# Optimization experiments

Measured on AMD Instinct MI355X. Metric: run time of the kernel, lower is better.

## Reference

```python
import jax, jax.numpy as jnp
import numpy as np

E = 2048        # embedding_dim
H = 16          # num_q_heads
G = 4           # group_size
HKV = H // G    # num_kv_heads = 4
D = E // H      # q_head_dim = 128
KVD = E // G    # kv_head_dim = 512
B, N = 2, 2048


def setup_inputs() -> dict:
    key = jax.random.key(0)
    ks = jax.random.split(key, 5)
    s = 0.02
    return {
        "x": jax.random.normal(ks[0], (B, N, E), jnp.float32),
        "Wq": jax.random.normal(ks[1], (E, E), jnp.float32) * s,
        "Wk": jax.random.normal(ks[2], (KVD, E), jnp.float32) * s,
        "Wv": jax.random.normal(ks[3], (KVD, E), jnp.float32) * s,
        "Wo": jax.random.normal(ks[4], (E, E), jnp.float32) * s,
    }


def reference(x, Wq, Wk, Wv, Wo):
    b, n, _ = x.shape
    # projections (nn.Linear: y = x @ W.T)
    q = x @ Wq.T                              # (b, n, E)
    k = x @ Wk.T                              # (b, n, KVD)
    v = x @ Wv.T                              # (b, n, KVD)
    # split heads: q -> b h n d with h=H, then (h g) -> g,h layout
    q = q.reshape(b, n, H, D).transpose(0, 2, 1, 3)          # b H n d
    q = q.reshape(b, HKV, G, n, D).transpose(0, 2, 1, 3, 4)  # b g h n d  (h=HKV)
    k = k.reshape(b, n, HKV, D).transpose(0, 2, 1, 3)        # b h s d
    v = v.reshape(b, n, HKV, D).transpose(0, 2, 1, 3)        # b h s d
    scale = 1.0 / jnp.sqrt(jnp.asarray(D, x.dtype))
    scores = jnp.einsum('bghnd,bhsd->bghns', q, k) * scale   # full score tensor
    scores = jax.nn.softmax(scores, axis=-1)
    # dropout p=0.0 -> identity
    o = jnp.einsum('bghns,bhsd->bghnd', scores, v)           # b g h n d
    # rearrange 'b g h n d -> b n (h g) d' then concat heads
    o = o.transpose(0, 3, 2, 1, 4).reshape(b, n, E)          # b n (h g) d -> b n E
    return o @ Wo.T
```

## Files before the change

### kernel.cpp

```cpp
#include <hip/hip_runtime.h>
#include <hip/hip_bf16.h>
#include <cstdint>
#include <cstddef>

using u16 = unsigned short;
typedef __bf16 bf16x8 __attribute__((ext_vector_type(8)));
typedef float f32x4 __attribute__((ext_vector_type(4)));
typedef float f32x16 __attribute__((ext_vector_type(16)));
typedef u16 u16x4 __attribute__((ext_vector_type(4)));
typedef u16 u16x8 __attribute__((ext_vector_type(8)));
typedef uint32_t u32x4 __attribute__((ext_vector_type(4)));

__device__ __forceinline__ u16 f2bf(float f) {
  uint32_t u = __builtin_bit_cast(uint32_t, f);
  u += 0x7FFFu + ((u >> 16) & 1u);
  return (u16)(u >> 16);
}

__device__ __forceinline__ void gld_lds16(const void* g, void* l) {
  __builtin_amdgcn_global_load_lds(
      (const __attribute__((address_space(1))) unsigned int*)g,
      (__attribute__((address_space(3))) unsigned int*)l, 16, 0, 0);
}

#define MFMA16(a, b, c) __builtin_amdgcn_mfma_f32_16x16x32_bf16((a), (b), (c), 0, 0, 0)
#define MFMA32(a, b, c) __builtin_amdgcn_mfma_f32_32x32x16_bf16((a), (b), (c), 0, 0, 0)

__device__ __forceinline__ uint32_t pkbf(float a, float b) {
  uint32_t d;
  asm("v_cvt_pk_bf16_f32 %0, %1, %2" : "=v"(d) : "v"(a), "v"(b));
  return d;
}
__device__ __forceinline__ void swap32(uint32_t& a, uint32_t& b) {
  asm volatile("v_permlane32_swap_b32 %0, %1" : "+v"(a), "+v"(b));
}

__global__ void cvt_kernel(const float* __restrict__ in, u16* __restrict__ out, int n4) {
  int i = blockIdx.x * blockDim.x + threadIdx.x;
  int stride = gridDim.x * blockDim.x;
  for (; i < n4; i += stride) {
    float4 v = reinterpret_cast<const float4*>(in)[i];
    u16x4 o;
    o[0] = f2bf(v.x); o[1] = f2bf(v.y); o[2] = f2bf(v.z); o[3] = f2bf(v.w);
    reinterpret_cast<u16x4*>(out)[i] = o;
  }
}

template <bool OUT_BF16>
__global__ __launch_bounds__(256) void gemm_bt(const u16* __restrict__ A,
                                               const u16* __restrict__ B,
                                               void* __restrict__ Cv,
                                               int M, int N, int K) {
  __shared__ __align__(16) u16 Ash[3][128 * 32];
  __shared__ __align__(16) u16 Bsh[3][128 * 32];
  const int tid = threadIdx.x;
  const int w = tid >> 6, lane = tid & 63, ql = lane & 15, g = lane >> 4;
  const int wr = w >> 1, wc = w & 1;
  const int m0 = blockIdx.y * 128, n0 = blockIdx.x * 128;
  const int srow = w * 16 + (lane >> 2);
  const int sk = (lane & 3) * 8;
  const u16* Abase = A + (size_t)(m0 + srow) * K + sk;
  const u16* Bbase = B + (size_t)(n0 + srow) * K + sk;

  f32x4 acc[4][4];
#pragma unroll
  for (int i = 0; i < 4; i++)
#pragma unroll
    for (int j = 0; j < 4; j++) acc[i][j] = f32x4{0.f, 0.f, 0.f, 0.f};

  auto stage = [&](int bi, int tile) {
    const int kt = tile * 32;
    gld_lds16(Abase + kt,                  &Ash[bi][w * 512]);
    gld_lds16(Abase + (size_t)64 * K + kt, &Ash[bi][2048 + w * 512]);
    gld_lds16(Bbase + kt,                  &Bsh[bi][w * 512]);
    gld_lds16(Bbase + (size_t)64 * K + kt, &Bsh[bi][2048 + w * 512]);
  };

  const int nt = K >> 5;
  stage(0, 0);
  stage(1, 1);
  asm volatile("s_waitcnt vmcnt(4)" ::: "memory");
  __builtin_amdgcn_sched_barrier(0);
  __builtin_amdgcn_s_barrier();
  __builtin_amdgcn_sched_barrier(0);

  int cur = 0;
  for (int t = 0; t < nt; ++t) {
    if (t + 2 < nt) {
      int stg = cur + 2; if (stg >= 3) stg -= 3;
      stage(stg, t + 2);
    }
    bf16x8 af[4], bfr[4];
#pragma unroll
    for (int i = 0; i < 4; i++)
      af[i] = *reinterpret_cast<const bf16x8*>(&Ash[cur][(wr * 64 + i * 16 + ql) * 32 + g * 8]);
#pragma unroll
    for (int j = 0; j < 4; j++)
      bfr[j] = *reinterpret_cast<const bf16x8*>(&Bsh[cur][(wc * 64 + j * 16 + ql) * 32 + g * 8]);
    __builtin_amdgcn_s_setprio(1);
#pragma unroll
    for (int i = 0; i < 4; i++)
#pragma unroll
      for (int j = 0; j < 4; j++)
        acc[i][j] = MFMA16(af[i], bfr[j], acc[i][j]);
    __builtin_amdgcn_s_setprio(0);
    if (t + 1 < nt) {
      if (t + 2 < nt) {
        asm volatile("s_waitcnt vmcnt(4)" ::: "memory");
      } else {
        asm volatile("s_waitcnt vmcnt(0)" ::: "memory");
      }
      __builtin_amdgcn_sched_barrier(0);
      __builtin_amdgcn_s_barrier();
      __builtin_amdgcn_sched_barrier(0);
    }
    cur = (cur == 2) ? 0 : cur + 1;
  }

#pragma unroll
  for (int i = 0; i < 4; i++)
#pragma unroll
    for (int j = 0; j < 4; j++)
#pragma unroll
      for (int r = 0; r < 4; r++) {
        const int row = m0 + wr * 64 + i * 16 + g * 4 + r;
        const int col = n0 + wc * 64 + j * 16 + ql;
        if constexpr (OUT_BF16)
          ((u16*)Cv)[(size_t)row * N + col] = f2bf(acc[i][j][r]);
        else
          ((float*)Cv)[(size_t)row * N + col] = acc[i][j][r];
      }
}

__global__ __launch_bounds__(256, 2) void attn_kernel(const u16* __restrict__ QKV,
                                                      u16* __restrict__ O) {
  __shared__ __align__(16) u16 Kb[2][64 * 128];
  __shared__ __align__(16) u16 Vb[2][2][128 * 32];
  const int tid = threadIdx.x, w = tid >> 6, lane = tid & 63;
  const int lq = lane & 31, hi = lane >> 5;
  const int qt = blockIdx.x;
  const int b = blockIdx.y >> 4, h = blockIdx.y & 15, hkv = h >> 2;
  const size_t rowb = (size_t)b * 2048;
  const int qbase = qt * 128 + w * 32;

  const u16* Kg = QKV + 2048 + hkv * 128;
  const u16* Vg = QKV + 2560 + hkv * 128;

  bf16x8 bq[8];
  {
    const u16* qp = QKV + (rowb + qbase + lq) * 3072 + h * 128 + hi * 8;
#pragma unroll
    for (int s5 = 0; s5 < 8; s5++)
      bq[s5] = *reinterpret_cast<const bf16x8*>(qp + s5 * 16);
  }

  const int dg = tid & 7, sl = tid >> 3;

  f32x16 oacc[4];
#pragma unroll
  for (int dt = 0; dt < 4; dt++)
#pragma unroll
    for (int i = 0; i < 16; i++) oacc[dt][i] = 0.f;
  float m = -INFINITY, l = 0.f;
  const float CEXP = 0.08838834764831845f * 1.4426950408889634f;

  auto stageK = [&](int pb2, int sbase) {
#pragma unroll
    for (int p = 0; p < 4; p++) {
      const int L = p * 2048 + tid * 8;
      const int s = L >> 7;
      const int gI = (L >> 3) & 15;
      gld_lds16(Kg + (rowb + sbase + s) * 3072 + ((gI ^ (s & 7)) << 3),
                &Kb[pb2][p * 2048 + w * 512]);
    }
  };
  auto writeV = [&](int pb2, const u16x8& a00, const u16x8& a01,
                    const u16x8& a10, const u16x8& a11) {
#pragma unroll
    for (int sh2 = 0; sh2 < 2; sh2++)
#pragma unroll
      for (int hf = 0; hf < 2; hf++) {
        const u16x8 v = sh2 ? (hf ? a11 : a10) : (hf ? a01 : a00);
#pragma unroll
        for (int j = 0; j < 8; j++) {
          const int d = dg * 16 + hf * 8 + j;
          const int key = ((d >> 1) ^ (d >> 4)) & 3;
          Vb[pb2][sh2][d * 32 + (sl ^ (key << 3))] = v[j];
        }
      }
  };

#define KFRAG(PB, SH, S5) \
  (*reinterpret_cast<const bf16x8*>(&Kb[PB][((SH)*32 + lq) * 128 + ((((S5)*2 + hi) ^ (lq & 7)) << 3)]))
#define VFRAG(PB, DT, SS) \
  (*reinterpret_cast<const bf16x8*>(&Vb[PB][(SS) >> 1][((DT)*32 + lq) * 32 + \
      ((((SS) & 1) * 16 + hi * 8) ^ (((((DT)*32 + lq) >> 1) ^ (((DT)*32 + lq) >> 4)) & 3) << 3)]))

  u16x8 v00, v01, v10, v11;
  {
    const u16* vp = Vg + (rowb + sl) * 3072 + dg * 16;
    v00 = *reinterpret_cast<const u16x8*>(vp);
    v01 = *reinterpret_cast<const u16x8*>(vp + 8);
    const u16* vp2 = vp + (size_t)32 * 3072;
    v10 = *reinterpret_cast<const u16x8*>(vp2);
    v11 = *reinterpret_cast<const u16x8*>(vp2 + 8);
  }
  stageK(0, 0);
  writeV(0, v00, v01, v10, v11);
  __syncthreads();

#pragma unroll 1
  for (int sb = 0; sb < 32; sb++) {
    const int pb = sb & 1;
    if (sb < 31) {
      const u16* vp = Vg + (rowb + (sb + 1) * 64 + sl) * 3072 + dg * 16;
      v00 = *reinterpret_cast<const u16x8*>(vp);
      v01 = *reinterpret_cast<const u16x8*>(vp + 8);
      const u16* vp2 = vp + (size_t)32 * 3072;
      v10 = *reinterpret_cast<const u16x8*>(vp2);
      v11 = *reinterpret_cast<const u16x8*>(vp2 + 8);
      stageK(pb ^ 1, (sb + 1) * 64);
    }

    f32x16 sc0, sc1;
#pragma unroll
    for (int i = 0; i < 16; i++) { sc0[i] = 0.f; sc1[i] = 0.f; }
    __builtin_amdgcn_s_setprio(1);
#pragma unroll
    for (int s5 = 0; s5 < 8; s5++) {
      sc0 = MFMA32(KFRAG(pb, 0, s5), bq[s5], sc0);
      sc1 = MFMA32(KFRAG(pb, 1, s5), bq[s5], sc1);
    }
    __builtin_amdgcn_s_setprio(0);

    float u[16];
#pragma unroll
    for (int i = 0; i < 16; i++) u[i] = fmaxf(sc0[i], sc1[i]);
#pragma unroll
    for (int i = 0; i < 8; i++) u[i] = fmaxf(u[i], u[i + 8]);
#pragma unroll
    for (int i = 0; i < 4; i++) u[i] = fmaxf(u[i], u[i + 4]);
    float mx = fmaxf(fmaxf(u[0], u[1]), fmaxf(u[2], u[3]));
    mx = fmaxf(mx, __shfl_xor(mx, 32));

    if (__any((mx - m) * CEXP > 8.0f)) {
      const float mn = fmaxf(m, mx);
      const float corr = exp2f((m - mn) * CEXP);
      l *= corr;
#pragma unroll
      for (int dt = 0; dt < 4; dt++)
#pragma unroll
        for (int i = 0; i < 16; i++) oacc[dt][i] *= corr;
      m = mn;
    }

    const float mC = m * CEXP;
    float e0[16], e1[16];
#pragma unroll
    for (int i = 0; i < 16; i++) {
      e0[i] = exp2f(fmaf(sc0[i], CEXP, -mC));
      e1[i] = exp2f(fmaf(sc1[i], CEXP, -mC));
    }
    float s[16];
#pragma unroll
    for (int i = 0; i < 16; i++) s[i] = e0[i] + e1[i];
#pragma unroll
    for (int i = 0; i < 8; i++) s[i] = s[i] + s[i + 8];
#pragma unroll
    for (int i = 0; i < 4; i++) s[i] = s[i] + s[i + 4];
    float ps = (s[0] + s[1]) + (s[2] + s[3]);
    ps += __shfl_xor(ps, 32);
    l += ps;

    bf16x8 pf0, pf1, pf2, pf3;
    {
      uint32_t a, bw;
      u32x4 f;
      a = pkbf(e0[0], e0[1]);  bw = pkbf(e0[4], e0[5]);  swap32(a, bw);
      f[0] = a; f[2] = bw;
      a = pkbf(e0[2], e0[3]);  bw = pkbf(e0[6], e0[7]);  swap32(a, bw);
      f[1] = a; f[3] = bw;
      pf0 = __builtin_bit_cast(bf16x8, f);
      a = pkbf(e0[8], e0[9]);  bw = pkbf(e0[12], e0[13]); swap32(a, bw);
      f[0] = a; f[2] = bw;
      a = pkbf(e0[10], e0[11]); bw = pkbf(e0[14], e0[15]); swap32(a, bw);
      f[1] = a; f[3] = bw;
      pf1 = __builtin_bit_cast(bf16x8, f);
      a = pkbf(e1[0], e1[1]);  bw = pkbf(e1[4], e1[5]);  swap32(a, bw);
      f[0] = a; f[2] = bw;
      a = pkbf(e1[2], e1[3]);  bw = pkbf(e1[6], e1[7]);  swap32(a, bw);
      f[1] = a; f[3] = bw;
      pf2 = __builtin_bit_cast(bf16x8, f);
      a = pkbf(e1[8], e1[9]);  bw = pkbf(e1[12], e1[13]); swap32(a, bw);
      f[0] = a; f[2] = bw;
      a = pkbf(e1[10], e1[11]); bw = pkbf(e1[14], e1[15]); swap32(a, bw);
      f[1] = a; f[3] = bw;
      pf3 = __builtin_bit_cast(bf16x8, f);
    }

    __builtin_amdgcn_s_setprio(1);
#pragma unroll
    for (int dt = 0; dt < 4; dt++) {
      oacc[dt] = MFMA32(VFRAG(pb, dt, 0), pf0, oacc[dt]);
      oacc[dt] = MFMA32(VFRAG(pb, dt, 1), pf1, oacc[dt]);
      oacc[dt] = MFMA32(VFRAG(pb, dt, 2), pf2, oacc[dt]);
      oacc[dt] = MFMA32(VFRAG(pb, dt, 3), pf3, oacc[dt]);
    }
    __builtin_amdgcn_s_setprio(0);

    if (sb < 31) writeV(pb ^ 1, v00, v01, v10, v11);
    __syncthreads();
  }

  const float rl = 1.0f / l;
  u16* ob = (w < 2) ? &Kb[w][0] : &Vb[w - 2][0][0];
#pragma unroll
  for (int dt = 0; dt < 4; dt++)
#pragma unroll
    for (int rq = 0; rq < 4; rq++) {
      u16x4 pv;
#pragma unroll
      for (int k = 0; k < 4; k++) pv[k] = f2bf(oacc[dt][rq * 4 + k] * rl);
      *reinterpret_cast<u16x4*>(&ob[lq * 136 + dt * 32 + rq * 8 + hi * 4]) = pv;
    }
  const int orow = lane >> 1, och = (lane & 1) * 64;
  u16* og = O + (rowb + qbase + orow) * 2048 + h * 128 + och;
#pragma unroll
  for (int t = 0; t < 8; t++) {
    u16x8 v = *reinterpret_cast<const u16x8*>(&ob[orow * 136 + och + t * 8]);
    *reinterpret_cast<u16x8*>(og + t * 8) = v;
  }
#undef KFRAG
#undef VFRAG
}

extern "C" void kernel_launch(void* const* d_in, const int* in_sizes, int n_in,
                              void* d_out, int out_size, void* d_ws, size_t ws_size,
                              hipStream_t stream) {
  (void)in_sizes; (void)n_in; (void)out_size;
  const float* x  = (const float*)d_in[0];
  const float* Wq = (const float*)d_in[1];
  const float* Wk = (const float*)d_in[2];
  const float* Wv = (const float*)d_in[3];
  const float* Wo = (const float*)d_in[4];

  if (ws_size < (size_t)(8388608 + 6291456 + 12582912) * 2) return;
  u16* xb  = (u16*)d_ws;
  u16* Wc  = xb + 8388608;
  u16* QKV = Wc + 6291456;
  u16* Ob  = xb;

  cvt_kernel<<<2048, 256, 0, stream>>>(x,  xb, 2097152);
  cvt_kernel<<<2048, 256, 0, stream>>>(Wq, Wc, 1048576);
  cvt_kernel<<<1024, 256, 0, stream>>>(Wk, Wc + 4194304, 262144);
  cvt_kernel<<<1024, 256, 0, stream>>>(Wv, Wc + 5242880, 262144);
  gemm_bt<true><<<dim3(24, 32), 256, 0, stream>>>(xb, Wc, (void*)QKV, 4096, 3072, 2048);
  cvt_kernel<<<2048, 256, 0, stream>>>(Wo, Wc, 1048576);
  attn_kernel<<<dim3(16, 32), 256, 0, stream>>>(QKV, Ob);
  gemm_bt<false><<<dim3(16, 32), 256, 0, stream>>>(Ob, Wc, d_out, 4096, 2048, 2048);
}
```

Before: 237.3 us.

## Software-pipeline PV MFMA, compute row sums via MFMA, fuse conversions, swizzle attention grid

The attention loop now defers each tile's P·V MFMAs to the next iteration, using a triple-buffered V in shared memory, so they overlap with the next QK^T and softmax. The softmax row-sum reduction and cross-lane shuffle are replaced by MFMAs against a ones vector that accumulate l in a register tile. The four fp32-to-bf16 conversion launches are merged into one kernel, and attention blocks are launched on a 1D grid with a swizzled mapping of (batch, head, q-tile) to improve K/V cache locality. The extra V buffer raises LDS use, which may cut occupancy, and the row sum now comes from bf16-rounded probabilities.

```diff
diff --git a/kernel.cpp b/kernel.cpp
--- a/kernel.cpp
+++ b/kernel.cpp
@@ -43,6 +43,24 @@
     u16x4 o;
     o[0] = f2bf(v.x); o[1] = f2bf(v.y); o[2] = f2bf(v.z); o[3] = f2bf(v.w);
     reinterpret_cast<u16x4*>(out)[i] = o;
+  }
+}
+
+__global__ void cvt4_kernel(const float* __restrict__ x, const float* __restrict__ Wq,
+                            const float* __restrict__ Wk, const float* __restrict__ Wv,
+                            u16* __restrict__ xb, u16* __restrict__ Wc) {
+  int i = blockIdx.x * blockDim.x + threadIdx.x;
+  int stride = gridDim.x * blockDim.x;
+  for (; i < 3670016; i += stride) {
+    const float* src; u16* dst; int off;
+    if (i < 2097152)      { src = x;  dst = xb;            off = i; }
+    else if (i < 3145728) { src = Wq; dst = Wc;            off = i - 2097152; }
+    else if (i < 3407872) { src = Wk; dst = Wc + 4194304;  off = i - 3145728; }
+    else                  { src = Wv; dst = Wc + 5242880;  off = i - 3407872; }
+    float4 v = reinterpret_cast<const float4*>(src)[off];
+    u16x4 o;
+    o[0] = f2bf(v.x); o[1] = f2bf(v.y); o[2] = f2bf(v.z); o[3] = f2bf(v.w);
+    reinterpret_cast<u16x4*>(dst)[off] = o;
   }
 }
 
@@ -135,11 +153,14 @@
 __global__ __launch_bounds__(256, 2) void attn_kernel(const u16* __restrict__ QKV,
                                                       u16* __restrict__ O) {
   __shared__ __align__(16) u16 Kb[2][64 * 128];
-  __shared__ __align__(16) u16 Vb[2][2][128 * 32];
+  __shared__ __align__(16) u16 Vb[3][2][128 * 32];
   const int tid = threadIdx.x, w = tid >> 6, lane = tid & 63;
   const int lq = lane & 31, hi = lane >> 5;
-  const int qt = blockIdx.x;
-  const int b = blockIdx.y >> 4, h = blockIdx.y & 15, hkv = h >> 2;
+  const int bid = blockIdx.x;
+  const int swz = (bid & 7) * 64 + (bid >> 3);
+  const int qt = swz & 15;
+  const int bh = swz >> 4;
+  const int b = bh >> 4, h = bh & 15, hkv = h >> 2;
   const size_t rowb = (size_t)b * 2048;
   const int qbase = qt * 128 + w * 32;
 
@@ -156,13 +177,18 @@
 
   const int dg = tid & 7, sl = tid >> 3;
 
-  f32x16 oacc[4];
+  f32x16 oacc[4], lacc;
 #pragma unroll
   for (int dt = 0; dt < 4; dt++)
 #pragma unroll
     for (int i = 0; i < 16; i++) oacc[dt][i] = 0.f;
-  float m = -INFINITY, l = 0.f;
+#pragma unroll
+  for (int i = 0; i < 16; i++) lacc[i] = 0.f;
+  float m = -INFINITY;
   const float CEXP = 0.08838834764831845f * 1.4426950408889634f;
+
+  const bf16x8 ones = __builtin_bit_cast(bf16x8,
+      u32x4{0x3F803F80u, 0x3F803F80u, 0x3F803F80u, 0x3F803F80u});
 
   auto stageK = [&](int pb2, int sbase) {
 #pragma unroll
@@ -174,7 +200,7 @@
                 &Kb[pb2][p * 2048 + w * 512]);
     }
   };
-  auto writeV = [&](int pb2, const u16x8& a00, const u16x8& a01,
+  auto writeV = [&](int vb3, const u16x8& a00, const u16x8& a01,
                     const u16x8& a10, const u16x8& a11) {
 #pragma unroll
     for (int sh2 = 0; sh2 < 2; sh2++)
@@ -185,15 +211,15 @@
         for (int j = 0; j < 8; j++) {
           const int d = dg * 16 + hf * 8 + j;
           const int key = ((d >> 1) ^ (d >> 4)) & 3;
-          Vb[pb2][sh2][d * 32 + (sl ^ (key << 3))] = v[j];
+          Vb[vb3][sh2][d * 32 + (sl ^ (key << 3))] = v[j];
         }
       }
   };
 
 #define KFRAG(PB, SH, S5) \
   (*reinterpret_cast<const bf16x8*>(&Kb[PB][((SH)*32 + lq) * 128 + ((((S5)*2 + hi) ^ (lq & 7)) << 3)]))
-#define VFRAG(PB, DT, SS) \
-  (*reinterpret_cast<const bf16x8*>(&Vb[PB][(SS) >> 1][((DT)*32 + lq) * 32 + \
+#define VFRAG(VB, DT, SS) \
+  (*reinterpret_cast<const bf16x8*>(&Vb[VB][(SS) >> 1][((DT)*32 + lq) * 32 + \
       ((((SS) & 1) * 16 + hi * 8) ^ (((((DT)*32 + lq) >> 1) ^ (((DT)*32 + lq) >> 4)) & 3) << 3)]))
 
   u16x8 v00, v01, v10, v11;
@@ -208,6 +234,9 @@
   stageK(0, 0);
   writeV(0, v00, v01, v10, v11);
   __syncthreads();
+
+  bf16x8 pf0, pf1, pf2, pf3;
+  int vprev = 2, vcur = 0, vnext = 1;
 
 #pragma unroll 1
   for (int sb = 0; sb < 32; sb++) {
@@ -233,6 +262,18 @@
     }
     __builtin_amdgcn_s_setprio(0);
 
+    if (sb) {
+      __builtin_amdgcn_s_setprio(1);
+#pragma unroll
+      for (int dt = 0; dt < 4; dt++) {
+        oacc[dt] = MFMA32(VFRAG(vprev, dt, 0), pf0, oacc[dt]);
+        oacc[dt] = MFMA32(VFRAG(vprev, dt, 1), pf1, oacc[dt]);
+        oacc[dt] = MFMA32(VFRAG(vprev, dt, 2), pf2, oacc[dt]);
+        oacc[dt] = MFMA32(VFRAG(vprev, dt, 3), pf3, oacc[dt]);
+      }
+      __builtin_amdgcn_s_setprio(0);
+    }
+
     float u[16];
 #pragma unroll
     for (int i = 0; i < 16; i++) u[i] = fmaxf(sc0[i], sc1[i]);
@@ -246,7 +287,8 @@
     if (__any((mx - m) * CEXP > 8.0f)) {
       const float mn = fmaxf(m, mx);
       const float corr = exp2f((m - mn) * CEXP);
-      l *= corr;
+#pragma unroll
+      for (int i = 0; i < 16; i++) lacc[i] *= corr;
 #pragma unroll
       for (int dt = 0; dt < 4; dt++)
 #pragma unroll
@@ -261,18 +303,6 @@
       e0[i] = exp2f(fmaf(sc0[i], CEXP, -mC));
       e1[i] = exp2f(fmaf(sc1[i], CEXP, -mC));
     }
-    float s[16];
-#pragma unroll
-    for (int i = 0; i < 16; i++) s[i] = e0[i] + e1[i];
-#pragma unroll
-    for (int i = 0; i < 8; i++) s[i] = s[i] + s[i + 8];
-#pragma unroll
-    for (int i = 0; i < 4; i++) s[i] = s[i] + s[i + 4];
-    float ps = (s[0] + s[1]) + (s[2] + s[3]);
-    ps += __shfl_xor(ps, 32);
-    l += ps;
-
-    bf16x8 pf0, pf1, pf2, pf3;
     {
       uint32_t a, bw;
       u32x4 f;
@@ -298,21 +328,31 @@
       pf3 = __builtin_bit_cast(bf16x8, f);
     }
 
+    lacc = MFMA32(ones, pf0, lacc);
+    lacc = MFMA32(ones, pf1, lacc);
+    lacc = MFMA32(ones, pf2, lacc);
+    lacc = MFMA32(ones, pf3, lacc);
+
+    if (sb < 31) writeV(vnext, v00, v01, v10, v11);
+    __syncthreads();
+
+    const int tmp = vprev; vprev = vcur; vcur = vnext; vnext = tmp;
+  }
+
+  {
     __builtin_amdgcn_s_setprio(1);
 #pragma unroll
     for (int dt = 0; dt < 4; dt++) {
-      oacc[dt] = MFMA32(VFRAG(pb, dt, 0), pf0, oacc[dt]);
-      oacc[dt] = MFMA32(VFRAG(pb, dt, 1), pf1, oacc[dt]);
-      oacc[dt] = MFMA32(VFRAG(pb, dt, 2), pf2, oacc[dt]);
-      oacc[dt] = MFMA32(VFRAG(pb, dt, 3), pf3, oacc[dt]);
+      oacc[dt] = MFMA32(VFRAG(vprev, dt, 0), pf0, oacc[dt]);
+      oacc[dt] = MFMA32(VFRAG(vprev, dt, 1), pf1, oacc[dt]);
+      oacc[dt] = MFMA32(VFRAG(vprev, dt, 2), pf2, oacc[dt]);
+      oacc[dt] = MFMA32(VFRAG(vprev, dt, 3), pf3, oacc[dt]);
     }
     __builtin_amdgcn_s_setprio(0);
-
-    if (sb < 31) writeV(pb ^ 1, v00, v01, v10, v11);
-    __syncthreads();
-  }
-
-  const float rl = 1.0f / l;
+  }
+  __syncthreads();
+
+  const float rl = 1.0f / lacc[0];
   u16* ob = (w < 2) ? &Kb[w][0] : &Vb[w - 2][0][0];
 #pragma unroll
   for (int dt = 0; dt < 4; dt++)
@@ -350,12 +390,9 @@
   u16* QKV = Wc + 6291456;
   u16* Ob  = xb;
 
-  cvt_kernel<<<2048, 256, 0, stream>>>(x,  xb, 2097152);
-  cvt_kernel<<<2048, 256, 0, stream>>>(Wq, Wc, 1048576);
-  cvt_kernel<<<1024, 256, 0, stream>>>(Wk, Wc + 4194304, 262144);
-  cvt_kernel<<<1024, 256, 0, stream>>>(Wv, Wc + 5242880, 262144);
+  cvt4_kernel<<<2048, 256, 0, stream>>>(x, Wq, Wk, Wv, xb, Wc);
   gemm_bt<true><<<dim3(24, 32), 256, 0, stream>>>(xb, Wc, (void*)QKV, 4096, 3072, 2048);
   cvt_kernel<<<2048, 256, 0, stream>>>(Wo, Wc, 1048576);
-  attn_kernel<<<dim3(16, 32), 256, 0, stream>>>(QKV, Ob);
+  attn_kernel<<<dim3(512), 256, 0, stream>>>(QKV, Ob);
   gemm_bt<false><<<dim3(16, 32), 256, 0, stream>>>(Ob, Wc, d_out, 4096, 2048, 2048);
 }
```

Measured after the change: 233.2 us. About the same (-1.7%).
